# Performance work log

Hardware: AMD Instinct MI355X
Metric: run time of the kernel (lower is better)

Reference implementation:

```python
import jax, jax.numpy as jnp
import numpy as np

B, H, Wd = 32, 64, 64
C_IN = 65            # ambient Lorentz dim (1 time + 64 space)
KH = KW = 3          # kernel
OUT = 256            # out_channels (ambient); linear space dim = 255
HCAT = (C_IN - 1) * KH * KW + 1  # 577
CURV = 1.0


def setup_inputs() -> dict:
    key = jax.random.key(0)
    k1, k2, k3 = jax.random.split(key, 3)
    # spatial (tangent-like) components, projected onto the hyperboloid
    v = jax.random.normal(k1, (B, H, Wd, C_IN - 1), dtype=jnp.float32) * 0.5
    t = jnp.sqrt(1.0 / CURV + jnp.sum(v * v, axis=-1, keepdims=True))
    x = jnp.concatenate([t, v], axis=-1)  # valid Lorentz points, (B,H,W,65)
    W = jax.random.normal(k2, (OUT - 1, HCAT), dtype=jnp.float32) * (1.0 / np.sqrt(HCAT))
    b = jnp.zeros((OUT - 1,), dtype=jnp.float32)
    return {"x": x, "W": W, "b": b}


def reference(x, W, b):
    c = CURV
    Bn, Hn, Wn, C = x.shape
    # 'SAME' padding with stride 1, kernel 3 -> pad 1 on each side, edge mode
    xp = jnp.pad(x, ((0, 0), (1, 1), (1, 1), (0, 0)), mode="edge")
    # im2col: stack the KH*KW shifted views -> (B, H, W, N, C)
    slabs = [xp[:, i:i + Hn, j:j + Wn, :] for i in range(KH) for j in range(KW)]
    patches = jnp.stack(slabs, axis=3)
    N = KH * KW
    # Lorentz direct concatenation (HCat):
    # time = sqrt(sum_i t_i^2 - (N-1)/c), space = concat of spatial parts
    t_cat = jnp.sqrt(jnp.sum(patches[..., 0] ** 2, axis=-1) - (N - 1) / c)
    sp = patches[..., 1:].reshape(Bn, Hn, Wn, N * (C - 1))
    h = jnp.concatenate([t_cat[..., None], sp], axis=-1)  # (B,H,W,577)
    # Hyperbolic linear (Lorentz fully-connected): space part is affine map,
    # time part restores the Lorentz constraint <y,y>_L = -1/c
    z = jnp.einsum("bhwi,oi->bhwo", h, W) + b  # (B,H,W,255)
    t_out = jnp.sqrt(1.0 / c + jnp.sum(z * z, axis=-1, keepdims=True))
    return jnp.concatenate([t_out, z], axis=-1)  # (B,H,W,256)
```

## Files before the change

### kernel.cpp

```cpp
#include <hip/hip_runtime.h>
#include <hip/hip_bf16.h>


#define CLAMP63(v) ((v) < 0 ? 0 : ((v) > 63 ? 63 : (v)))

typedef __attribute__((ext_vector_type(8))) short short8;
typedef __attribute__((ext_vector_type(4))) float floatx4;

__device__ __forceinline__ void gl2lds16(const void* g, void* l) {
  __builtin_amdgcn_global_load_lds(
      (const __attribute__((address_space(1))) void*)g,
      (__attribute__((address_space(3))) void*)l, 16, 0, 0);
}

__global__ void prep_x(const float* __restrict__ x, __hip_bfloat16* __restrict__ xs) {
  int idx = blockIdx.x * 256 + threadIdx.x;
  int p = idx >> 3, g = idx & 7;
  const float* src = x + (size_t)p * 65 + 1 + g * 8;
  __align__(16) __hip_bfloat16 tmp[8];
#pragma unroll
  for (int i = 0; i < 8; ++i) tmp[i] = __float2bfloat16(src[i]);
  *(short8*)(xs + (size_t)idx * 8) = *(const short8*)tmp;
}

__global__ void prep_w(const float* __restrict__ W, const float* __restrict__ b,
                       __hip_bfloat16* __restrict__ Wb, float* __restrict__ Wt0,
                       float* __restrict__ bp) {
  int n = blockIdx.x;
  for (int k = threadIdx.x; k < 576; k += 256)
    Wb[n * 576 + k] = __float2bfloat16((n < 255) ? W[n * 577 + 1 + k] : 0.f);
  if (threadIdx.x == 0) {
    Wt0[n] = (n < 255) ? W[n * 577] : 0.f;
    bp[n]  = (n < 255) ? b[n] : 0.f;
  }
}

#define STAGE(IT, BUF)                                                          \
  do {                                                                          \
    const int nbr_ = (IT) >> 1;                                                 \
    const int dy_ = nbr_ / 3 - 1, dx_ = nbr_ % 3 - 1;                           \
    const int c0_ = ((IT) & 1) * 32;                                            \
    _Pragma("unroll")                                                           \
    for (int q = 0; q < 2; ++q) {                                               \
      int y2 = CLAMP63(a_by[q] + dy_);                                          \
      int x2 = CLAMP63(a_bx[q] + dx_);                                          \
      const __hip_bfloat16* src =                                               \
          xs + (size_t)((a_bb[q] * 64 + y2) * 64 + x2) * 64 + c0_ + w * 8;      \
      gl2lds16(src, Ab + (BUF) * 4096 + (w * 2 + q) * 512);                     \
    }                                                                           \
    _Pragma("unroll")                                                           \
    for (int p = 0; p < 4; ++p)                                                 \
      gl2lds16(b_src[p] + (IT) * 32, Bb + (BUF) * 8192 + (w * 4 + p) * 512);    \
  } while (0)

__launch_bounds__(256, 2)
__global__ void hypconv_main(const float* __restrict__ x,
                             const __hip_bfloat16* __restrict__ xs,
                             const __hip_bfloat16* __restrict__ Wb,
                             const float* __restrict__ Wt0,
                             const float* __restrict__ bp,
                             float* __restrict__ out) {
  __shared__ __align__(16) char smem[49152];
  __shared__ float tc_lds[128];
  ushort* Ab = (ushort*)smem;
  ushort* Bb = (ushort*)(smem + 16384);
  float* zbuf = (float*)smem;

  const int tid = threadIdx.x;
  const int w = tid >> 6, lane = tid & 63;
  const int quad = lane >> 4, ln = lane & 15;
  const int pix_base = blockIdx.x * 128;
  const int m_off = (w >> 1) * 64, n_off = (w & 1) * 128;

  int a_bx[2], a_by[2], a_bb[2];
#pragma unroll
  for (int q = 0; q < 2; ++q) {
    int pix = pix_base + q * 64 + lane;
    a_bx[q] = pix & 63; a_by[q] = (pix >> 6) & 63; a_bb[q] = pix >> 12;
  }
  const __hip_bfloat16* b_src[4];
#pragma unroll
  for (int p = 0; p < 4; ++p)
    b_src[p] = Wb + (size_t)(p * 64 + lane) * 576 + w * 8;

  floatx4 acc[4][8];
#pragma unroll
  for (int mf = 0; mf < 4; ++mf)
#pragma unroll
    for (int nf = 0; nf < 8; ++nf)
      acc[mf][nf] = (floatx4){0.f, 0.f, 0.f, 0.f};

  STAGE(0, 0);

  if (tid < 128) {
    int pix = pix_base + tid;
    int bx = pix & 63, by = (pix >> 6) & 63, bb = pix >> 12;
    float s = 0.f;
#pragma unroll
    for (int dy = -1; dy <= 1; ++dy) {
      int y2 = CLAMP63(by + dy);
#pragma unroll
      for (int dx = -1; dx <= 1; ++dx) {
        int x2 = CLAMP63(bx + dx);
        float t = x[(size_t)((bb * 64 + y2) * 64 + x2) * 65];
        s += t * t;
      }
    }
    tc_lds[tid] = sqrtf(s - 8.0f);
  }

  for (int it = 0; it < 18; ++it) {
    __syncthreads();
    if (it < 17) STAGE(it + 1, (it + 1) & 1);
    const ushort* Ar = Ab + (it & 1) * 4096;
    const ushort* Br = Bb + (it & 1) * 8192;
    short8 af[4], bfr[8];
#pragma unroll
    for (int mf = 0; mf < 4; ++mf)
      af[mf] = *(const short8*)&Ar[(quad * 128 + m_off + mf * 16 + ln) * 8];
#pragma unroll
    for (int nf = 0; nf < 8; ++nf)
      bfr[nf] = *(const short8*)&Br[(quad * 256 + n_off + nf * 16 + ln) * 8];
#pragma unroll
    for (int mf = 0; mf < 4; ++mf)
#pragma unroll
      for (int nf = 0; nf < 8; ++nf)
        acc[mf][nf] = __builtin_amdgcn_mfma_f32_16x16x32_bf16(af[mf], bfr[nf], acc[mf][nf], 0, 0, 0);
  }

  __syncthreads();
  float wn[8], bnv[8];
#pragma unroll
  for (int nf = 0; nf < 8; ++nf) {
    int n = n_off + nf * 16 + ln;
    wn[nf] = Wt0[n];
    bnv[nf] = bp[n];
  }

#pragma unroll
  for (int mf = 0; mf < 4; ++mf) {
#pragma unroll
    for (int r = 0; r < 4; ++r) {
      float tcv = tc_lds[m_off + mf * 16 + quad * 4 + r];
      int lr = (w >> 1) * 16 + quad * 4 + r;
#pragma unroll
      for (int nf = 0; nf < 8; ++nf) {
        float z = acc[mf][nf][r] + bnv[nf] + tcv * wn[nf];
        zbuf[lr * 256 + ((1 + n_off + nf * 16 + ln) & 255)] = z;
      }
    }
    __syncthreads();
#pragma unroll
    for (int rr = 0; rr < 8; ++rr) {
      int lr = w * 8 + rr;
      float4 v = *(const float4*)&zbuf[lr * 256 + lane * 4];
      float ss = v.x * v.x + v.y * v.y + v.z * v.z + v.w * v.w;
      ss += __shfl_xor(ss, 1, 64);
      ss += __shfl_xor(ss, 2, 64);
      ss += __shfl_xor(ss, 4, 64);
      ss += __shfl_xor(ss, 8, 64);
      ss += __shfl_xor(ss, 16, 64);
      ss += __shfl_xor(ss, 32, 64);
      float tout = sqrtf(1.0f + ss);
      if (lane == 0) v.x = tout;
      int m = (lr >> 4) * 64 + mf * 16 + (lr & 15);
      *(float4*)&out[(size_t)(pix_base + m) * 256 + lane * 4] = v;
    }
    if (mf < 3) __syncthreads();
  }
}

extern "C" void kernel_launch(void* const* d_in, const int* in_sizes, int n_in,
                              void* d_out, int out_size, void* d_ws, size_t ws_size,
                              hipStream_t stream) {
  const float* x = (const float*)d_in[0];
  const float* W = (const float*)d_in[1];
  const float* b = (const float*)d_in[2];
  float* out = (float*)d_out;
  char* ws = (char*)d_ws;

  __hip_bfloat16* xs  = (__hip_bfloat16*)(ws);
  __hip_bfloat16* Wb  = (__hip_bfloat16*)(ws + 16777216);
  float*          Wt0 = (float*)(ws + 17072128);
  float*          bp  = (float*)(ws + 17073152);

  prep_x<<<4096, 256, 0, stream>>>(x, xs);
  prep_w<<<256,  256, 0, stream>>>(W, b, Wb, Wt0, bp);
  hypconv_main<<<1024, 256, 0, stream>>>(x, xs, Wb, Wt0, bp, out);
}
```

Measured before the change: 224.8 us.

## Split GEMM block across eight waves with smaller per-wave tiles

Doubles the threads per block to 512 and gives each wave a 64x64 output sub-tile instead of 64x128, roughly halving the accumulator registers per wave so more waves can be resident. The A and B staging loads are redistributed across the eight waves. The time-component squares are now precomputed in prep_x, so the main kernel reads them contiguously instead of with a strided gather from x. The zbuf row stride is padded to 260 to reduce LDS bank conflicts. In exchange, each wave does more LDS fragment reads per MFMA, and the larger blocks add more barrier synchronisation.

Measured after the change: 221.9 us. Within noise of the previous version (-1.3%).

```diff
diff --git a/kernel.cpp b/kernel.cpp
--- a/kernel.cpp
+++ b/kernel.cpp
@@ -13,7 +13,8 @@
       (__attribute__((address_space(3))) void*)l, 16, 0, 0);
 }
 
-__global__ void prep_x(const float* __restrict__ x, __hip_bfloat16* __restrict__ xs) {
+__global__ void prep_x(const float* __restrict__ x, __hip_bfloat16* __restrict__ xs,
+                       float* __restrict__ tsq) {
   int idx = blockIdx.x * 256 + threadIdx.x;
   int p = idx >> 3, g = idx & 7;
   const float* src = x + (size_t)p * 65 + 1 + g * 8;
@@ -21,6 +22,7 @@
 #pragma unroll
   for (int i = 0; i < 8; ++i) tmp[i] = __float2bfloat16(src[i]);
   *(short8*)(xs + (size_t)idx * 8) = *(const short8*)tmp;
+  if (g == 0) { float t = x[(size_t)p * 65]; tsq[p] = t * t; }
 }
 
 __global__ void prep_w(const float* __restrict__ W, const float* __restrict__ b,
@@ -40,21 +42,17 @@
     const int nbr_ = (IT) >> 1;                                                 \
     const int dy_ = nbr_ / 3 - 1, dx_ = nbr_ % 3 - 1;                           \
     const int c0_ = ((IT) & 1) * 32;                                            \
+    int y2_ = CLAMP63(a_by + dy_);                                              \
+    int x2_ = CLAMP63(a_bx + dx_);                                              \
+    gl2lds16(xs + (size_t)((a_bb * 64 + y2_) * 64 + x2_) * 64 + c0_ + a_kg * 8, \
+             Ab + (BUF) * 4096 + w * 512);                                      \
     _Pragma("unroll")                                                           \
-    for (int q = 0; q < 2; ++q) {                                               \
-      int y2 = CLAMP63(a_by[q] + dy_);                                          \
-      int x2 = CLAMP63(a_bx[q] + dx_);                                          \
-      const __hip_bfloat16* src =                                               \
-          xs + (size_t)((a_bb[q] * 64 + y2) * 64 + x2) * 64 + c0_ + w * 8;      \
-      gl2lds16(src, Ab + (BUF) * 4096 + (w * 2 + q) * 512);                     \
-    }                                                                           \
-    _Pragma("unroll")                                                           \
-    for (int p = 0; p < 4; ++p)                                                 \
-      gl2lds16(b_src[p] + (IT) * 32, Bb + (BUF) * 8192 + (w * 4 + p) * 512);    \
+    for (int j = 0; j < 2; ++j)                                                 \
+      gl2lds16(b_src[j] + (IT) * 32, Bb + (BUF) * 8192 + (w * 2 + j) * 512);    \
   } while (0)
 
-__launch_bounds__(256, 2)
-__global__ void hypconv_main(const float* __restrict__ x,
+__launch_bounds__(512, 4)
+__global__ void hypconv_main(const float* __restrict__ tsq,
                              const __hip_bfloat16* __restrict__ xs,
                              const __hip_bfloat16* __restrict__ Wb,
                              const float* __restrict__ Wt0,
@@ -70,24 +68,23 @@
   const int w = tid >> 6, lane = tid & 63;
   const int quad = lane >> 4, ln = lane & 15;
   const int pix_base = blockIdx.x * 128;
-  const int m_off = (w >> 1) * 64, n_off = (w & 1) * 128;
+  const int m_off = (w >> 2) * 64, n_off = (w & 3) * 64;
 
-  int a_bx[2], a_by[2], a_bb[2];
+  const int a_kg = w >> 1;
+  int apix = pix_base + (w & 1) * 64 + lane;
+  const int a_bx = apix & 63, a_by = (apix >> 6) & 63, a_bb = apix >> 12;
+  const __hip_bfloat16* b_src[2];
 #pragma unroll
-  for (int q = 0; q < 2; ++q) {
-    int pix = pix_base + q * 64 + lane;
-    a_bx[q] = pix & 63; a_by[q] = (pix >> 6) & 63; a_bb[q] = pix >> 12;
+  for (int j = 0; j < 2; ++j) {
+    int c = w * 2 + j;
+    b_src[j] = Wb + (size_t)((c & 3) * 64 + lane) * 576 + (c >> 2) * 8;
   }
-  const __hip_bfloat16* b_src[4];
-#pragma unroll
-  for (int p = 0; p < 4; ++p)
-    b_src[p] = Wb + (size_t)(p * 64 + lane) * 576 + w * 8;
 
-  floatx4 acc[4][8];
+  floatx4 acc[4][4];
 #pragma unroll
   for (int mf = 0; mf < 4; ++mf)
 #pragma unroll
-    for (int nf = 0; nf < 8; ++nf)
+    for (int nf = 0; nf < 4; ++nf)
       acc[mf][nf] = (floatx4){0.f, 0.f, 0.f, 0.f};
 
   STAGE(0, 0);
@@ -102,8 +99,7 @@
 #pragma unroll
       for (int dx = -1; dx <= 1; ++dx) {
         int x2 = CLAMP63(bx + dx);
-        float t = x[(size_t)((bb * 64 + y2) * 64 + x2) * 65];
-        s += t * t;
+        s += tsq[(bb * 64 + y2) * 64 + x2];
       }
     }
     tc_lds[tid] = sqrtf(s - 8.0f);
@@ -114,24 +110,24 @@
     if (it < 17) STAGE(it + 1, (it + 1) & 1);
     const ushort* Ar = Ab + (it & 1) * 4096;
     const ushort* Br = Bb + (it & 1) * 8192;
-    short8 af[4], bfr[8];
+    short8 af[4], bfr[4];
 #pragma unroll
     for (int mf = 0; mf < 4; ++mf)
       af[mf] = *(const short8*)&Ar[(quad * 128 + m_off + mf * 16 + ln) * 8];
 #pragma unroll
-    for (int nf = 0; nf < 8; ++nf)
+    for (int nf = 0; nf < 4; ++nf)
       bfr[nf] = *(const short8*)&Br[(quad * 256 + n_off + nf * 16 + ln) * 8];
 #pragma unroll
     for (int mf = 0; mf < 4; ++mf)
 #pragma unroll
-      for (int nf = 0; nf < 8; ++nf)
+      for (int nf = 0; nf < 4; ++nf)
         acc[mf][nf] = __builtin_amdgcn_mfma_f32_16x16x32_bf16(af[mf], bfr[nf], acc[mf][nf], 0, 0, 0);
   }
 
   __syncthreads();
-  float wn[8], bnv[8];
+  float wn[4], bnv[4];
 #pragma unroll
-  for (int nf = 0; nf < 8; ++nf) {
+  for (int nf = 0; nf < 4; ++nf) {
     int n = n_off + nf * 16 + ln;
     wn[nf] = Wt0[n];
     bnv[nf] = bp[n];
@@ -142,18 +138,18 @@
 #pragma unroll
     for (int r = 0; r < 4; ++r) {
       float tcv = tc_lds[m_off + mf * 16 + quad * 4 + r];
-      int lr = (w >> 1) * 16 + quad * 4 + r;
+      int lr = (w >> 2) * 16 + quad * 4 + r;
 #pragma unroll
-      for (int nf = 0; nf < 8; ++nf) {
+      for (int nf = 0; nf < 4; ++nf) {
         float z = acc[mf][nf][r] + bnv[nf] + tcv * wn[nf];
-        zbuf[lr * 256 + ((1 + n_off + nf * 16 + ln) & 255)] = z;
+        zbuf[lr * 260 + ((1 + n_off + nf * 16 + ln) & 255)] = z;
       }
     }
     __syncthreads();
 #pragma unroll
-    for (int rr = 0; rr < 8; ++rr) {
-      int lr = w * 8 + rr;
-      float4 v = *(const float4*)&zbuf[lr * 256 + lane * 4];
+    for (int rr = 0; rr < 4; ++rr) {
+      int lr = w * 4 + rr;
+      float4 v = *(const float4*)&zbuf[lr * 260 + lane * 4];
       float ss = v.x * v.x + v.y * v.y + v.z * v.z + v.w * v.w;
       ss += __shfl_xor(ss, 1, 64);
       ss += __shfl_xor(ss, 2, 64);
@@ -183,8 +179,9 @@
   __hip_bfloat16* Wb  = (__hip_bfloat16*)(ws + 16777216);
   float*          Wt0 = (float*)(ws + 17072128);
   float*          bp  = (float*)(ws + 17073152);
+  float*          tsq = (float*)(ws + 17074176);
 
-  prep_x<<<4096, 256, 0, stream>>>(x, xs);
+  prep_x<<<4096, 256, 0, stream>>>(x, xs, tsq);
   prep_w<<<256,  256, 0, stream>>>(W, b, Wb, Wt0, bp);
-  hypconv_main<<<1024, 256, 0, stream>>>(x, xs, Wb, Wt0, bp, out);
+  hypconv_main<<<1024, 512, 0, stream>>>(tsq, xs, Wb, Wt0, bp, out);
 }
```
